# Optimization experiments

Hardware: AMD Instinct MI355X
Metric: run time of the kernel (lower is better)

Reference implementation:

```python
import jax, jax.numpy as jnp
import numpy as np

E = 320000   # num edges / messages
N = 10000    # num target nodes (dim_size)
C = 256      # in_channels == out_channels


def setup_inputs() -> dict:
    key = jax.random.key(0)
    k1, k2, k3, k4, k5, k6 = jax.random.split(key, 6)
    s = 1.0 / np.sqrt(C)  # torch Linear default init bound
    return {
        "from_tensor": jax.random.normal(k1, (E, C), dtype=jnp.float32),
        "to_index": jax.random.randint(k2, (E,), 0, N),
        "dim_size": N,
        "W1": jax.random.uniform(k3, (C, C), jnp.float32, -s, s),
        "b1": jax.random.uniform(k4, (C,), jnp.float32, -s, s),
        "W2": jax.random.uniform(k5, (C, C), jnp.float32, -s, s),
        "b2": jax.random.uniform(k6, (C,), jnp.float32, -s, s),
    }


def reference(from_tensor, to_index, dim_size, W1, b1, W2, b2):
    # InterMessage with transform_scatter=True, num_layers=2, reduction='mean':
    # message = MLP(from_tensor); out = scatter_mean(message, to_index, dim_size)
    m = jax.nn.relu(from_tensor @ W1 + b1)          # [E, C]
    m = jax.nn.relu(m @ W2 + b2)                    # [E, C]
    sums = jax.ops.segment_sum(m, to_index, num_segments=dim_size)  # [N, C]
    cnt = jax.ops.segment_sum(jnp.ones((m.shape[0], 1), m.dtype), to_index,
                              num_segments=dim_size)                # [N, 1]
    # scatter-mean: empty segments produce 0 (matches torch_scatter 'mean')
    return jnp.where(cnt > 0, sums / jnp.maximum(cnt, 1.0), 0.0)
```

## Files before the change

### kernel.cpp

```cpp
#include <hip/hip_runtime.h>

#define NUM_E 320000
#define NUM_N 10000
#define PADC 32

typedef __attribute__((ext_vector_type(8))) short bf16x8;
typedef __attribute__((ext_vector_type(4))) float f32x4;

__device__ __forceinline__ short f2bf(float f) {
  unsigned u = __builtin_bit_cast(unsigned, f);
  u += 0x7FFFu + ((u >> 16) & 1u);
  return (short)(u >> 16);
}

__device__ __forceinline__ unsigned pack2bf(float x, float y) {
  unsigned ux = __builtin_bit_cast(unsigned, x);
  unsigned uy = __builtin_bit_cast(unsigned, y);
  ux += 0x7FFFu + ((ux >> 16) & 1u);
  uy += 0x7FFFu + ((uy >> 16) & 1u);
  return __builtin_amdgcn_perm(uy, ux, 0x07060302u);
}

__global__ __launch_bounds__(256) void zero_repack_k(
    const float* __restrict__ W1, const float* __restrict__ W2,
    short* __restrict__ Wp, int* __restrict__ cntA, float* __restrict__ out) {
  const int gtid = blockIdx.x * 256 + threadIdx.x;
  const int gsz = gridDim.x * 256;
  for (int i = gtid; i < 640000; i += gsz)
    reinterpret_cast<float4*>(out)[i] = make_float4(0.f, 0.f, 0.f, 0.f);
  for (int i = gtid; i < NUM_N * PADC / 4; i += gsz)
    reinterpret_cast<int4*>(cntA)[i] = make_int4(0, 0, 0, 0);
  if (gtid < 16384) {
    const float* W = (gtid & 8192) ? W2 : W1;
    int r = gtid & 8191;
    short* dst = Wp + (gtid >> 13) * 65536 + r * 8;
    int j = r >> 9;
    int s = (r >> 6) & 7;
    int lane = r & 63;
    int n = j * 16 + (lane & 15);
    int k0 = s * 32 + (lane >> 4) * 8;
    short tmp[8];
#pragma unroll
    for (int e = 0; e < 8; ++e) tmp[e] = f2bf(W[(k0 + e) * 256 + n]);
#pragma unroll
    for (int e = 0; e < 8; ++e) dst[e] = tmp[e];
  }
}

__global__ __launch_bounds__(256) void hist_k(const int* __restrict__ idx,
                                              int* __restrict__ cntA) {
  int e = blockIdx.x * 256 + threadIdx.x;
  if (e < NUM_E) atomicAdd(&cntA[idx[e] * PADC], 1);
}

__global__ __launch_bounds__(256) void scan_k(const int* __restrict__ cntA,
                                              int* __restrict__ fillP,
                                              float* __restrict__ inv) {
  __shared__ int part[256];
  int t = threadIdx.x;
  int base = t * 40;
  int local[40];
  int s = 0;
#pragma unroll
  for (int i = 0; i < 40; ++i) {
    int n = base + i;
    int c = (n < NUM_N) ? cntA[n * PADC] : 0;
    local[i] = s;
    s += c;
  }
  part[t] = s;
  __syncthreads();
  for (int off = 1; off < 256; off <<= 1) {
    int tmp = 0;
    if (t >= off) tmp = part[t - off];
    __syncthreads();
    if (t >= off) part[t] += tmp;
    __syncthreads();
  }
  int ebase = (t == 0) ? 0 : part[t - 1];
#pragma unroll
  for (int i = 0; i < 40; ++i) {
    int n = base + i;
    if (n < NUM_N) {
      fillP[n * PADC] = ebase + local[i];
      int c = cntA[n * PADC];
      inv[n] = (c > 0) ? 1.0f / (float)c : 0.0f;
    }
  }
}

__global__ __launch_bounds__(256) void scatter_k(const int* __restrict__ idx,
                                                 int* __restrict__ fillP,
                                                 int* __restrict__ sorted) {
  int e = blockIdx.x * 256 + threadIdx.x;
  if (e < NUM_E) {
    int ix = idx[e];
    int pos = atomicAdd(&fillP[ix * PADC], 1);
    sorted[pos] = e;
  }
}

__global__ __launch_bounds__(256, 4) void fused_mlp_gather(
    const float* __restrict__ X, const int* __restrict__ idx,
    const int* __restrict__ sorted,
    const short* __restrict__ Wp1, const short* __restrict__ Wp2,
    const float* __restrict__ b1, const float* __restrict__ b2,
    const float* __restrict__ inv, float* __restrict__ out) {
  __shared__ __align__(16) short Xl[64][264];
  __shared__ int idxl[64];
  __shared__ int se[64];
  __shared__ int segLo[64];
  __shared__ int segN[64];
  __shared__ int nsegS;

  const int tid = threadIdx.x;
  const int wave = tid >> 6;
  const int lane = tid & 63;
  const int q = lane >> 4;
  const int m = lane & 15;
  const int row0 = blockIdx.x * 64;

  if (tid < 64) {
    int e = sorted[row0 + tid];
    se[tid] = e;
    idxl[tid] = idx[e];
  }
  __syncthreads();

  for (int i = tid; i < 64 * 64; i += 256) {
    int r = i >> 6, c4 = i & 63;
    const float4 v = reinterpret_cast<const float4*>(X + (size_t)se[r] * 256)[c4];
    uint2 p;
    p.x = pack2bf(v.x, v.y);
    p.y = pack2bf(v.z, v.w);
    *reinterpret_cast<uint2*>(&Xl[r][c4 * 4]) = p;
  }
  __syncthreads();

  if (wave == 0) {
    bool flag = (lane == 0) || (idxl[lane] != idxl[lane - 1]);
    unsigned long long mask = __ballot(flag);
    if (lane == 0) nsegS = (int)__popcll(mask);
    if (flag) {
      int sidx = (int)__popcll(mask & ((1ull << lane) - 1ull));
      segLo[sidx] = lane;
      segN[sidx] = idxl[lane];
    }
  }

  f32x4 acc[4][4];
#pragma unroll
  for (int mi = 0; mi < 4; ++mi)
#pragma unroll
    for (int nj = 0; nj < 4; ++nj) acc[mi][nj] = (f32x4)0.0f;

#pragma unroll
  for (int s = 0; s < 8; ++s) {
    bf16x8 a[4], b[4];
#pragma unroll
    for (int mi = 0; mi < 4; ++mi)
      a[mi] = *reinterpret_cast<const bf16x8*>(&Xl[mi * 16 + m][s * 32 + q * 8]);
#pragma unroll
    for (int nj = 0; nj < 4; ++nj)
      b[nj] = *reinterpret_cast<const bf16x8*>(
          Wp1 + (size_t)(((wave * 4 + nj) * 8 + s) * 64 + lane) * 8);
#pragma unroll
    for (int mi = 0; mi < 4; ++mi)
#pragma unroll
      for (int nj = 0; nj < 4; ++nj)
        acc[mi][nj] = __builtin_amdgcn_mfma_f32_16x16x32_bf16(a[mi], b[nj],
                                                              acc[mi][nj], 0, 0, 0);
  }
  __syncthreads();

  float bias1[4];
#pragma unroll
  for (int nj = 0; nj < 4; ++nj) bias1[nj] = b1[wave * 64 + nj * 16 + m];
#pragma unroll
  for (int mi = 0; mi < 4; ++mi)
#pragma unroll
    for (int nj = 0; nj < 4; ++nj)
#pragma unroll
      for (int r4 = 0; r4 < 4; ++r4) {
        float v = fmaxf(acc[mi][nj][r4] + bias1[nj], 0.0f);
        Xl[mi * 16 + q * 4 + r4][wave * 64 + nj * 16 + m] = f2bf(v);
      }
  __syncthreads();

#pragma unroll
  for (int mi = 0; mi < 4; ++mi)
#pragma unroll
    for (int nj = 0; nj < 4; ++nj) acc[mi][nj] = (f32x4)0.0f;

#pragma unroll
  for (int s = 0; s < 8; ++s) {
    bf16x8 a[4], b[4];
#pragma unroll
    for (int mi = 0; mi < 4; ++mi)
      a[mi] = *reinterpret_cast<const bf16x8*>(&Xl[mi * 16 + m][s * 32 + q * 8]);
#pragma unroll
    for (int nj = 0; nj < 4; ++nj)
      b[nj] = *reinterpret_cast<const bf16x8*>(
          Wp2 + (size_t)(((wave * 4 + nj) * 8 + s) * 64 + lane) * 8);
#pragma unroll
    for (int mi = 0; mi < 4; ++mi)
#pragma unroll
      for (int nj = 0; nj < 4; ++nj)
        acc[mi][nj] = __builtin_amdgcn_mfma_f32_16x16x32_bf16(a[mi], b[nj],
                                                              acc[mi][nj], 0, 0, 0);
  }

  float bias2[4];
#pragma unroll
  for (int nj = 0; nj < 4; ++nj) bias2[nj] = b2[wave * 64 + nj * 16 + m];
#pragma unroll
  for (int mi = 0; mi < 4; ++mi)
#pragma unroll
    for (int nj = 0; nj < 4; ++nj)
#pragma unroll
      for (int r4 = 0; r4 < 4; ++r4)
        acc[mi][nj][r4] = fmaxf(acc[mi][nj][r4] + bias2[nj], 0.0f);

  int nseg = nsegS;
  for (int s = 0; s < nseg; ++s) {
    int lo = segLo[s];
    int hi = (s + 1 < nseg) ? segLo[s + 1] : 64;
    int node = segN[s];
    float sum[4] = {0.0f, 0.0f, 0.0f, 0.0f};
#pragma unroll
    for (int mi = 0; mi < 4; ++mi)
#pragma unroll
      for (int r4 = 0; r4 < 4; ++r4) {
        int row = mi * 16 + q * 4 + r4;
        float msk = (row >= lo && row < hi) ? 1.0f : 0.0f;
#pragma unroll
        for (int nj = 0; nj < 4; ++nj) sum[nj] = fmaf(msk, acc[mi][nj][r4], sum[nj]);
      }
    float scale = inv[node];
#pragma unroll
    for (int nj = 0; nj < 4; ++nj) {
      float v = sum[nj];
      v += __shfl_xor(v, 16, 64);
      v += __shfl_xor(v, 32, 64);
      if (q == 0 && v != 0.0f)
        atomicAdd(&out[(size_t)node * 256 + wave * 64 + nj * 16 + m], v * scale);
    }
  }
}

extern "C" void kernel_launch(void* const* d_in, const int* in_sizes, int n_in,
                              void* d_out, int out_size, void* d_ws, size_t ws_size,
                              hipStream_t stream) {
  const float* X   = (const float*)d_in[0];
  const int*   idx = (const int*)d_in[1];
  const float* W1  = (const float*)d_in[3];
  const float* b1  = (const float*)d_in[4];
  const float* W2  = (const float*)d_in[5];
  const float* b2  = (const float*)d_in[6];
  float* out = (float*)d_out;

  char* ws = (char*)d_ws;
  short* Wp    = (short*)(ws);
  int*   cntA  = (int*)(ws + 262144);
  int*   fillP = (int*)(ws + 1542144);
  float* inv   = (float*)(ws + 2822144);
  int*   sorted = cntA;

  zero_repack_k<<<2048, 256, 0, stream>>>(W1, W2, Wp, cntA, out);
  hist_k<<<(NUM_E + 255) / 256, 256, 0, stream>>>(idx, cntA);
  scan_k<<<1, 256, 0, stream>>>(cntA, fillP, inv);
  scatter_k<<<(NUM_E + 255) / 256, 256, 0, stream>>>(idx, fillP, sorted);
  fused_mlp_gather<<<NUM_E / 64, 256, 0, stream>>>(
      X, idx, sorted, Wp, Wp + 65536, b1, b2, inv, out);
}
```

Before: 588.1 us.

## Batch gathered row loads, use wave-atomic allocation instead of serial scan

```diff
diff --git a/kernel.cpp b/kernel.cpp
--- a/kernel.cpp
+++ b/kernel.cpp
@@ -23,9 +23,11 @@
 
 __global__ __launch_bounds__(256) void zero_repack_k(
     const float* __restrict__ W1, const float* __restrict__ W2,
-    short* __restrict__ Wp, int* __restrict__ cntA, float* __restrict__ out) {
+    short* __restrict__ Wp, int* __restrict__ cntA, int* __restrict__ cursor,
+    float* __restrict__ out) {
   const int gtid = blockIdx.x * 256 + threadIdx.x;
   const int gsz = gridDim.x * 256;
+  if (gtid == 0) *cursor = 0;
   for (int i = gtid; i < 640000; i += gsz)
     reinterpret_cast<float4*>(out)[i] = make_float4(0.f, 0.f, 0.f, 0.f);
   for (int i = gtid; i < NUM_N * PADC / 4; i += gsz)
@@ -53,39 +55,26 @@
   if (e < NUM_E) atomicAdd(&cntA[idx[e] * PADC], 1);
 }
 
-__global__ __launch_bounds__(256) void scan_k(const int* __restrict__ cntA,
-                                              int* __restrict__ fillP,
-                                              float* __restrict__ inv) {
-  __shared__ int part[256];
-  int t = threadIdx.x;
-  int base = t * 40;
-  int local[40];
-  int s = 0;
-#pragma unroll
-  for (int i = 0; i < 40; ++i) {
-    int n = base + i;
-    int c = (n < NUM_N) ? cntA[n * PADC] : 0;
-    local[i] = s;
-    s += c;
-  }
-  part[t] = s;
-  __syncthreads();
-  for (int off = 1; off < 256; off <<= 1) {
-    int tmp = 0;
-    if (t >= off) tmp = part[t - off];
-    __syncthreads();
-    if (t >= off) part[t] += tmp;
-    __syncthreads();
-  }
-  int ebase = (t == 0) ? 0 : part[t - 1];
-#pragma unroll
-  for (int i = 0; i < 40; ++i) {
-    int n = base + i;
-    if (n < NUM_N) {
-      fillP[n * PADC] = ebase + local[i];
-      int c = cntA[n * PADC];
-      inv[n] = (c > 0) ? 1.0f / (float)c : 0.0f;
-    }
+__global__ __launch_bounds__(256) void alloc_k(const int* __restrict__ cntA,
+                                               int* __restrict__ fillP,
+                                               float* __restrict__ inv,
+                                               int* __restrict__ cursor) {
+  int n = blockIdx.x * 256 + threadIdx.x;
+  int lane = threadIdx.x & 63;
+  int c = (n < NUM_N) ? cntA[n * PADC] : 0;
+  int pre = c;
+#pragma unroll
+  for (int off = 1; off < 64; off <<= 1) {
+    int v = __shfl_up(pre, off, 64);
+    if (lane >= off) pre += v;
+  }
+  int tot = __shfl(pre, 63, 64);
+  int base = 0;
+  if (lane == 63) base = atomicAdd(cursor, tot);
+  base = __shfl(base, 63, 64);
+  if (n < NUM_N) {
+    fillP[n * PADC] = base + pre - c;
+    inv[n] = (c > 0) ? 1.0f / (float)c : 0.0f;
   }
 }
 
@@ -100,7 +89,7 @@
   }
 }
 
-__global__ __launch_bounds__(256, 4) void fused_mlp_gather(
+__global__ __launch_bounds__(256, 3) void fused_mlp_gather(
     const float* __restrict__ X, const int* __restrict__ idx,
     const int* __restrict__ sorted,
     const short* __restrict__ Wp1, const short* __restrict__ Wp2,
@@ -127,12 +116,20 @@
   }
   __syncthreads();
 
-  for (int i = tid; i < 64 * 64; i += 256) {
+  float4 vbuf[16];
+#pragma unroll
+  for (int k = 0; k < 16; ++k) {
+    int i = tid + k * 256;
     int r = i >> 6, c4 = i & 63;
-    const float4 v = reinterpret_cast<const float4*>(X + (size_t)se[r] * 256)[c4];
+    vbuf[k] = reinterpret_cast<const float4*>(X + (size_t)se[r] * 256)[c4];
+  }
+#pragma unroll
+  for (int k = 0; k < 16; ++k) {
+    int i = tid + k * 256;
+    int r = i >> 6, c4 = i & 63;
     uint2 p;
-    p.x = pack2bf(v.x, v.y);
-    p.y = pack2bf(v.z, v.w);
+    p.x = pack2bf(vbuf[k].x, vbuf[k].y);
+    p.y = pack2bf(vbuf[k].z, vbuf[k].w);
     *reinterpret_cast<uint2*>(&Xl[r][c4 * 4]) = p;
   }
   __syncthreads();
@@ -164,12 +161,14 @@
     for (int nj = 0; nj < 4; ++nj)
       b[nj] = *reinterpret_cast<const bf16x8*>(
           Wp1 + (size_t)(((wave * 4 + nj) * 8 + s) * 64 + lane) * 8);
+    __builtin_amdgcn_s_setprio(1);
 #pragma unroll
     for (int mi = 0; mi < 4; ++mi)
 #pragma unroll
       for (int nj = 0; nj < 4; ++nj)
         acc[mi][nj] = __builtin_amdgcn_mfma_f32_16x16x32_bf16(a[mi], b[nj],
                                                               acc[mi][nj], 0, 0, 0);
+    __builtin_amdgcn_s_setprio(0);
   }
   __syncthreads();
 
@@ -202,12 +201,14 @@
     for (int nj = 0; nj < 4; ++nj)
       b[nj] = *reinterpret_cast<const bf16x8*>(
           Wp2 + (size_t)(((wave * 4 + nj) * 8 + s) * 64 + lane) * 8);
+    __builtin_amdgcn_s_setprio(1);
 #pragma unroll
     for (int mi = 0; mi < 4; ++mi)
 #pragma unroll
       for (int nj = 0; nj < 4; ++nj)
         acc[mi][nj] = __builtin_amdgcn_mfma_f32_16x16x32_bf16(a[mi], b[nj],
                                                               acc[mi][nj], 0, 0, 0);
+    __builtin_amdgcn_s_setprio(0);
   }
 
   float bias2[4];
@@ -260,15 +261,16 @@
   float* out = (float*)d_out;
 
   char* ws = (char*)d_ws;
-  short* Wp    = (short*)(ws);
-  int*   cntA  = (int*)(ws + 262144);
-  int*   fillP = (int*)(ws + 1542144);
-  float* inv   = (float*)(ws + 2822144);
+  short* Wp     = (short*)(ws);
+  int*   cntA   = (int*)(ws + 262144);
+  int*   fillP  = (int*)(ws + 1542144);
+  float* inv    = (float*)(ws + 2822144);
+  int*   cursor = (int*)(ws + 2863104);
   int*   sorted = cntA;
 
-  zero_repack_k<<<2048, 256, 0, stream>>>(W1, W2, Wp, cntA, out);
+  zero_repack_k<<<2048, 256, 0, stream>>>(W1, W2, Wp, cntA, cursor, out);
   hist_k<<<(NUM_E + 255) / 256, 256, 0, stream>>>(idx, cntA);
-  scan_k<<<1, 256, 0, stream>>>(cntA, fillP, inv);
+  alloc_k<<<40, 256, 0, stream>>>(cntA, fillP, inv, cursor);
   scatter_k<<<(NUM_E + 255) / 256, 256, 0, stream>>>(idx, fillP, sorted);
   fused_mlp_gather<<<NUM_E / 64, 256, 0, stream>>>(
       X, idx, sorted, Wp, Wp + 65536, b1, b2, inv, out);
```

Result: faster. 545.3 us (-7.3%).
